# Kernel optimization log

Hardware: AMD Instinct MI355X
Metric: run time of the kernel (lower is better)

The kernel has to match this reference:

```python
import jax, jax.numpy as jnp
import numpy as np

ALPHA = 0.2  # LeakyReLU negative slope


def _gat_layer(h, dst, adj, w, a_in, a_out, b):
    # h: [N, F_in], dst: [N, K] int (edge (i,k): i -> dst[i,k]), adj: [N, K]
    hid = h @ w                      # [N, D]
    s_in = hid @ a_in                # [N]  (attention applied to source-node half)
    s_out = hid @ a_out              # [N]  (attention applied to dest-node half)
    # edge scores, grouped per source node (matches view(-1, num_neighs) softmax)
    e = jax.nn.leaky_relu(s_in[:, None] + s_out[dst], ALPHA)   # [N, K]
    # torch code detaches attention (Variable(..., requires_grad=False))
    att = jax.lax.stop_gradient(jax.nn.softmax(e, axis=1))     # [N, K]
    w_edge = adj * att                                          # [N, K]
    # SpMM: out[i] = sum_k w_edge[i,k] * hid[dst[i,k]]
    out = jnp.einsum('nk,nkd->nd', w_edge, hid[dst]) + b        # [N, D]
    return out


def setup_inputs() -> dict:
    key = jax.random.key(0)
    ks = jax.random.split(key, 12)
    N, K, F, H, O = 100000, 16, 128, 128, 128
    stdv1 = 1.0 / np.sqrt(H)
    stdv2 = 1.0 / np.sqrt(O)
    u = lambda k, shp, s: jax.random.uniform(k, shp, jnp.float32, -s, s)
    return {
        'x': jax.random.normal(ks[0], (N, F), jnp.float32),
        'dst_idx': jax.random.randint(ks[1], (N, K), 0, N),
        'adj_vals': jax.random.uniform(ks[2], (N, K), jnp.float32),
        'w1': u(ks[3], (F, H), stdv1),
        'a_in1': jax.random.normal(ks[4], (H,), jnp.float32) * (1.414 / np.sqrt(H)),
        'a_out1': jax.random.normal(ks[5], (H,), jnp.float32) * (1.414 / np.sqrt(H)),
        'b1': u(ks[6], (H,), stdv1),
        'w2': u(ks[7], (H, O), stdv2),
        'a_in2': jax.random.normal(ks[8], (O,), jnp.float32) * (1.414 / np.sqrt(O)),
        'a_out2': jax.random.normal(ks[9], (O,), jnp.float32) * (1.414 / np.sqrt(O)),
        'b2': u(ks[10], (O,), stdv2),
    }


def reference(x, dst_idx, adj_vals, w1, a_in1, a_out1, b1, w2, a_in2, a_out2, b2):
    h = jax.nn.relu(_gat_layer(x, dst_idx, adj_vals, w1, a_in1, a_out1, b1))
    h = jax.nn.relu(_gat_layer(h, dst_idx, adj_vals, w2, a_in2, a_out2, b2))
    return h
```

## Files before the change

### kernel.cpp

```cpp
#include <hip/hip_runtime.h>

#define ALPHA 0.2f
#define LDA 136

typedef short bf16x8 __attribute__((ext_vector_type(8)));
typedef float f32x4  __attribute__((ext_vector_type(4)));

static __device__ __forceinline__ float bf2f(unsigned short u) {
    union { unsigned int i; float f; } v; v.i = ((unsigned int)u) << 16; return v.f;
}
static __device__ __forceinline__ unsigned short f2bf(float f) {
    union { float f; unsigned int i; } v; v.f = f;
    unsigned int x = v.i;
    return (unsigned short)((x + 0x7fffu + ((x >> 16) & 1u)) >> 16);
}

__global__ __launch_bounds__(256)
void prep_wT_kernel(const float* __restrict__ w1, const float* __restrict__ w2,
                    unsigned short* __restrict__ wT1, unsigned short* __restrict__ wT2)
{
    __shared__ unsigned short wL[128 * 130];
    const float* w = blockIdx.x ? w2 : w1;
    unsigned short* wT = blockIdx.x ? wT2 : wT1;
    const int tid = threadIdx.x;

    for (int i = 0; i < 16; i++) {
        int e = tid + i * 256;
        int k = e >> 5, c0 = (e & 31) * 4;
        float4 v = *(const float4*)&w[k * 128 + c0];
        wL[(c0 + 0) * 130 + k] = f2bf(v.x);
        wL[(c0 + 1) * 130 + k] = f2bf(v.y);
        wL[(c0 + 2) * 130 + k] = f2bf(v.z);
        wL[(c0 + 3) * 130 + k] = f2bf(v.w);
    }
    __syncthreads();
    for (int i = 0; i < 8; i++) {
        int e = tid + i * 256;
        int c = e >> 4, k0 = (e & 15) * 8;
        ushort4 a, b;
        a.x = wL[c * 130 + k0 + 0]; a.y = wL[c * 130 + k0 + 1];
        a.z = wL[c * 130 + k0 + 2]; a.w = wL[c * 130 + k0 + 3];
        b.x = wL[c * 130 + k0 + 4]; b.y = wL[c * 130 + k0 + 5];
        b.z = wL[c * 130 + k0 + 6]; b.w = wL[c * 130 + k0 + 7];
        *(ushort4*)&wT[c * 128 + k0]     = a;
        *(ushort4*)&wT[c * 128 + k0 + 4] = b;
    }
}

template <bool SRC_BF>
__global__ __launch_bounds__(256)
void gemm_score_mfma(const void* __restrict__ srcv,
                     const unsigned short* __restrict__ wT,
                     const float* __restrict__ a_in,
                     const float* __restrict__ a_out,
                     unsigned short* __restrict__ hid,
                     float* __restrict__ s_in,
                     float* __restrict__ s_out,
                     int n)
{
    __shared__ short As[64 * LDA];
    __shared__ short Bs[128 * LDA];
    __shared__ float aS[2][128];

    const int tid = threadIdx.x;
    const int rbase = blockIdx.x * 64;

    if (tid < 128) { aS[0][tid] = a_in[tid]; aS[1][tid] = a_out[tid]; }

    if (SRC_BF) {
        const unsigned short* src = (const unsigned short*)srcv;
        #pragma unroll
        for (int i = 0; i < 8; i++) {
            int e = tid + i * 256;
            int r = e >> 5, c4 = (e & 31) * 4;
            int gr = rbase + r;
            ushort4 v;
            if (gr < n) v = *(const ushort4*)&src[(size_t)gr * 128 + c4];
            else { v.x = v.y = v.z = v.w = 0; }
            *(ushort4*)&As[r * LDA + c4] = v;
        }
    } else {
        const float* src = (const float*)srcv;
        #pragma unroll
        for (int i = 0; i < 8; i++) {
            int e = tid + i * 256;
            int r = e >> 5, c4 = (e & 31) * 4;
            int gr = rbase + r;
            ushort4 u;
            if (gr < n) {
                float4 v = *(const float4*)&src[(size_t)gr * 128 + c4];
                u.x = f2bf(v.x); u.y = f2bf(v.y); u.z = f2bf(v.z); u.w = f2bf(v.w);
            } else { u.x = u.y = u.z = u.w = 0; }
            *(ushort4*)&As[r * LDA + c4] = u;
        }
    }
    #pragma unroll
    for (int i = 0; i < 8; i++) {
        int e = tid + i * 256;
        int nr = e >> 4, j = (e & 15) * 8;
        int4 v = *(const int4*)&wT[nr * 128 + j];
        *(int4*)&Bs[nr * LDA + j] = v;
    }
    __syncthreads();

    const int lane = tid & 63;
    const int wv = tid >> 6;
    const int m = lane & 15;
    const int q = lane >> 4;

    f32x4 acc[8];
    #pragma unroll
    for (int t = 0; t < 8; t++) acc[t] = (f32x4){0.f, 0.f, 0.f, 0.f};

    const short* Abase = &As[(wv * 16 + m) * LDA + q * 8];
    const short* Bbase = &Bs[m * LDA + q * 8];

    #pragma unroll
    for (int ks = 0; ks < 4; ks++) {
        bf16x8 aF = *(const bf16x8*)(Abase + ks * 32);
        #pragma unroll
        for (int t = 0; t < 8; t++) {
            bf16x8 bF = *(const bf16x8*)(Bbase + t * 16 * LDA + ks * 32);
            acc[t] = __builtin_amdgcn_mfma_f32_16x16x32_bf16(aF, bF, acc[t], 0, 0, 0);
        }
    }

    float pin[4] = {0.f, 0.f, 0.f, 0.f}, pout[4] = {0.f, 0.f, 0.f, 0.f};
    #pragma unroll
    for (int t = 0; t < 8; t++) {
        float ai = aS[0][t * 16 + m];
        float ao = aS[1][t * 16 + m];
        #pragma unroll
        for (int r = 0; r < 4; r++) {
            pin[r]  += acc[t][r] * ai;
            pout[r] += acc[t][r] * ao;
        }
    }
    #pragma unroll
    for (int msk = 8; msk >= 1; msk >>= 1) {
        #pragma unroll
        for (int r = 0; r < 4; r++) {
            pin[r]  += __shfl_xor(pin[r],  msk);
            pout[r] += __shfl_xor(pout[r], msk);
        }
    }
    if (m == 0) {
        #pragma unroll
        for (int r = 0; r < 4; r++) {
            int g = rbase + wv * 16 + q * 4 + r;
            if (g < n) { s_in[g] = pin[r]; s_out[g] = pout[r]; }
        }
    }

    #pragma unroll
    for (int t = 0; t < 8; t++)
        #pragma unroll
        for (int r = 0; r < 4; r++)
            As[(wv * 16 + q * 4 + r) * LDA + t * 16 + m] = (short)f2bf(acc[t][r]);
    __syncthreads();
    #pragma unroll
    for (int i = 0; i < 4; i++) {
        int e = tid + i * 256;
        int r = e >> 4, j = (e & 15) * 8;
        int gr = rbase + r;
        if (gr < n) {
            int4 v = *(const int4*)&As[r * LDA + j];
            *(int4*)&hid[(size_t)gr * 128 + j] = v;
        }
    }
}

template <bool FINAL>
__global__ __launch_bounds__(256)
void gat_aggregate_kernel(const unsigned short* __restrict__ hid,
                          const float* __restrict__ s_in,
                          const float* __restrict__ s_out,
                          const int* __restrict__ dst,
                          const float* __restrict__ adj,
                          const float* __restrict__ bias,
                          void* __restrict__ outv,
                          int n)
{
    const int lane = threadIdx.x & 63;
    const int node = (blockIdx.x * 256 + threadIdx.x) >> 6;
    if (node >= n) return;

    float sc = -1e30f;
    int dk = 0;
    float av = 0.f;
    if (lane < 16) {
        int ei = node * 16 + lane;
        dk = dst[ei];
        av = adj[ei];
        float e = s_in[node] + s_out[dk];
        sc = (e > 0.f) ? e : ALPHA * e;
    }
    float m = sc;
    #pragma unroll
    for (int msk = 8; msk >= 1; msk >>= 1) m = fmaxf(m, __shfl_xor(m, msk));
    float p = (lane < 16) ? __expf(sc - m) : 0.f;
    float s = p;
    #pragma unroll
    for (int msk = 8; msk >= 1; msk >>= 1) s += __shfl_xor(s, msk);
    float wk = (lane < 16) ? av * p / s : 0.f;

    const int sub = lane >> 4;
    const int oct = lane & 15;
    int   gdk[4];
    float gwk[4];
    #pragma unroll
    for (int j = 0; j < 4; j++) {
        gdk[j] = __shfl(dk, 4 * j + sub);
        gwk[j] = __shfl(wk, 4 * j + sub);
    }

    float acc[8];
    #pragma unroll
    for (int i = 0; i < 8; i++) acc[i] = 0.f;
    #pragma unroll
    for (int j = 0; j < 4; j++) {
        bf16x8 hv = *(const bf16x8*)&hid[(size_t)gdk[j] * 128 + oct * 8];
        float wj = gwk[j];
        #pragma unroll
        for (int i = 0; i < 8; i++)
            acc[i] += wj * bf2f((unsigned short)hv[i]);
    }
    #pragma unroll
    for (int i = 0; i < 8; i++) {
        acc[i] += __shfl_xor(acc[i], 16);
        acc[i] += __shfl_xor(acc[i], 32);
    }

    if (lane < 16) {
        float4 b0 = *(const float4*)&bias[oct * 8];
        float4 b1 = *(const float4*)&bias[oct * 8 + 4];
        float o[8];
        o[0] = fmaxf(acc[0] + b0.x, 0.f); o[1] = fmaxf(acc[1] + b0.y, 0.f);
        o[2] = fmaxf(acc[2] + b0.z, 0.f); o[3] = fmaxf(acc[3] + b0.w, 0.f);
        o[4] = fmaxf(acc[4] + b1.x, 0.f); o[5] = fmaxf(acc[5] + b1.y, 0.f);
        o[6] = fmaxf(acc[6] + b1.z, 0.f); o[7] = fmaxf(acc[7] + b1.w, 0.f);

        const size_t obase = (size_t)node * 128 + oct * 8;
        if (FINAL) {
            float* of = (float*)outv;
            *(float4*)&of[obase]     = make_float4(o[0], o[1], o[2], o[3]);
            *(float4*)&of[obase + 4] = make_float4(o[4], o[5], o[6], o[7]);
        } else {
            unsigned short* oh = (unsigned short*)outv;
            ushort4 u0, u1;
            u0.x = f2bf(o[0]); u0.y = f2bf(o[1]); u0.z = f2bf(o[2]); u0.w = f2bf(o[3]);
            u1.x = f2bf(o[4]); u1.y = f2bf(o[5]); u1.z = f2bf(o[6]); u1.w = f2bf(o[7]);
            *(ushort4*)&oh[obase]     = u0;
            *(ushort4*)&oh[obase + 4] = u1;
        }
    }
}

extern "C" void kernel_launch(void* const* d_in, const int* in_sizes, int n_in,
                              void* d_out, int out_size, void* d_ws, size_t ws_size,
                              hipStream_t stream)
{
    const float* x      = (const float*)d_in[0];
    const int*   dst    = (const int*)d_in[1];
    const float* adj    = (const float*)d_in[2];
    const float* w1     = (const float*)d_in[3];
    const float* a_in1  = (const float*)d_in[4];
    const float* a_out1 = (const float*)d_in[5];
    const float* b1     = (const float*)d_in[6];
    const float* w2     = (const float*)d_in[7];
    const float* a_in2  = (const float*)d_in[8];
    const float* a_out2 = (const float*)d_in[9];
    const float* b2     = (const float*)d_in[10];

    const int N = in_sizes[0] / 128;

    unsigned short* hid   = (unsigned short*)d_ws;
    float*          s_in  = (float*)(hid + (size_t)N * 128);
    float*          s_out = s_in + N;
    unsigned short* wT1   = (unsigned short*)(s_out + N);
    unsigned short* wT2   = wT1 + 128 * 128;
    unsigned short* h1    = (unsigned short*)d_out + out_size;

    dim3 blk(256);
    dim3 ggrid((N + 63) / 64);
    dim3 agrid((N + 3) / 4);

    prep_wT_kernel<<<2, blk, 0, stream>>>(w1, w2, wT1, wT2);

    gemm_score_mfma<false><<<ggrid, blk, 0, stream>>>(x,  wT1, a_in1, a_out1,
                                                      hid, s_in, s_out, N);
    gat_aggregate_kernel<false><<<agrid, blk, 0, stream>>>(hid, s_in, s_out, dst,
                                                           adj, b1, h1, N);
    gemm_score_mfma<true><<<ggrid, blk, 0, stream>>>(h1, wT2, a_in2, a_out2,
                                                     hid, s_in, s_out, N);
    gat_aggregate_kernel<true><<<agrid, blk, 0, stream>>>(hid, s_in, s_out, dst,
                                                          adj, b2, d_out, N);
}
```

Before: 276.0 us.

## Load GEMM operands directly from global into MFMA registers, drop LDS staging

The GEMM kernel no longer stages the input rows and the transposed weight into shared memory. Each lane loads its A fragments straight from global memory into registers, and B fragments come from the small L2-resident weight buffer. This cuts LDS use from about 52KB to about 17KB per block, which allows higher occupancy and removes a barrier and the LDS round trip. The cost is redundant global/L2 reads of the weight by every wave. The weight transpose prep kernel is also rewritten to spread the work over 32 blocks without shared memory.

```diff
diff --git a/kernel.cpp b/kernel.cpp
--- a/kernel.cpp
+++ b/kernel.cpp
@@ -15,36 +15,23 @@
     return (unsigned short)((x + 0x7fffu + ((x >> 16) & 1u)) >> 16);
 }
 
-__global__ __launch_bounds__(256)
+__global__ __launch_bounds__(128)
 void prep_wT_kernel(const float* __restrict__ w1, const float* __restrict__ w2,
                     unsigned short* __restrict__ wT1, unsigned short* __restrict__ wT2)
 {
-    __shared__ unsigned short wL[128 * 130];
-    const float* w = blockIdx.x ? w2 : w1;
-    unsigned short* wT = blockIdx.x ? wT2 : wT1;
-    const int tid = threadIdx.x;
-
-    for (int i = 0; i < 16; i++) {
-        int e = tid + i * 256;
-        int k = e >> 5, c0 = (e & 31) * 4;
-        float4 v = *(const float4*)&w[k * 128 + c0];
-        wL[(c0 + 0) * 130 + k] = f2bf(v.x);
-        wL[(c0 + 1) * 130 + k] = f2bf(v.y);
-        wL[(c0 + 2) * 130 + k] = f2bf(v.z);
-        wL[(c0 + 3) * 130 + k] = f2bf(v.w);
-    }
-    __syncthreads();
-    for (int i = 0; i < 8; i++) {
-        int e = tid + i * 256;
-        int c = e >> 4, k0 = (e & 15) * 8;
-        ushort4 a, b;
-        a.x = wL[c * 130 + k0 + 0]; a.y = wL[c * 130 + k0 + 1];
-        a.z = wL[c * 130 + k0 + 2]; a.w = wL[c * 130 + k0 + 3];
-        b.x = wL[c * 130 + k0 + 4]; b.y = wL[c * 130 + k0 + 5];
-        b.z = wL[c * 130 + k0 + 6]; b.w = wL[c * 130 + k0 + 7];
-        *(ushort4*)&wT[c * 128 + k0]     = a;
-        *(ushort4*)&wT[c * 128 + k0 + 4] = b;
-    }
+    const int b = blockIdx.x;
+    const float* w = (b >> 4) ? w2 : w1;
+    unsigned short* wT = (b >> 4) ? wT2 : wT1;
+    const int k0 = (b & 15) * 8;
+    const int c = threadIdx.x;
+
+    ushort4 u0, u1;
+    u0.x = f2bf(w[(k0 + 0) * 128 + c]); u0.y = f2bf(w[(k0 + 1) * 128 + c]);
+    u0.z = f2bf(w[(k0 + 2) * 128 + c]); u0.w = f2bf(w[(k0 + 3) * 128 + c]);
+    u1.x = f2bf(w[(k0 + 4) * 128 + c]); u1.y = f2bf(w[(k0 + 5) * 128 + c]);
+    u1.z = f2bf(w[(k0 + 6) * 128 + c]); u1.w = f2bf(w[(k0 + 7) * 128 + c]);
+    *(ushort4*)&wT[c * 128 + k0]     = u0;
+    *(ushort4*)&wT[c * 128 + k0 + 4] = u1;
 }
 
 template <bool SRC_BF>
@@ -58,70 +45,57 @@
                      float* __restrict__ s_out,
                      int n)
 {
-    __shared__ short As[64 * LDA];
-    __shared__ short Bs[128 * LDA];
+    __shared__ short Es[64 * LDA];
     __shared__ float aS[2][128];
 
-    const int tid = threadIdx.x;
+    const int tid  = threadIdx.x;
+    const int lane = tid & 63;
+    const int wv   = tid >> 6;
+    const int m    = lane & 15;
+    const int q    = lane >> 4;
     const int rbase = blockIdx.x * 64;
+    const int row   = rbase + wv * 16 + m;
+    const bool rok  = (row < n);
 
     if (tid < 128) { aS[0][tid] = a_in[tid]; aS[1][tid] = a_out[tid]; }
-
+    __syncthreads();
+
+    bf16x8 aF[4];
     if (SRC_BF) {
         const unsigned short* src = (const unsigned short*)srcv;
-        #pragma unroll
-        for (int i = 0; i < 8; i++) {
-            int e = tid + i * 256;
-            int r = e >> 5, c4 = (e & 31) * 4;
-            int gr = rbase + r;
-            ushort4 v;
-            if (gr < n) v = *(const ushort4*)&src[(size_t)gr * 128 + c4];
-            else { v.x = v.y = v.z = v.w = 0; }
-            *(ushort4*)&As[r * LDA + c4] = v;
-        }
+        const unsigned short* p = &src[(size_t)row * 128 + q * 8];
+        #pragma unroll
+        for (int ks = 0; ks < 4; ks++)
+            aF[ks] = rok ? *(const bf16x8*)(p + ks * 32) : (bf16x8){0,0,0,0,0,0,0,0};
     } else {
         const float* src = (const float*)srcv;
-        #pragma unroll
-        for (int i = 0; i < 8; i++) {
-            int e = tid + i * 256;
-            int r = e >> 5, c4 = (e & 31) * 4;
-            int gr = rbase + r;
-            ushort4 u;
-            if (gr < n) {
-                float4 v = *(const float4*)&src[(size_t)gr * 128 + c4];
-                u.x = f2bf(v.x); u.y = f2bf(v.y); u.z = f2bf(v.z); u.w = f2bf(v.w);
-            } else { u.x = u.y = u.z = u.w = 0; }
-            *(ushort4*)&As[r * LDA + c4] = u;
-        }
-    }
-    #pragma unroll
-    for (int i = 0; i < 8; i++) {
-        int e = tid + i * 256;
-        int nr = e >> 4, j = (e & 15) * 8;
-        int4 v = *(const int4*)&wT[nr * 128 + j];
-        *(int4*)&Bs[nr * LDA + j] = v;
-    }
-    __syncthreads();
-
-    const int lane = tid & 63;
-    const int wv = tid >> 6;
-    const int m = lane & 15;
-    const int q = lane >> 4;
+        const float* p = &src[(size_t)row * 128 + q * 8];
+        #pragma unroll
+        for (int ks = 0; ks < 4; ks++) {
+            if (rok) {
+                float4 v0 = *(const float4*)(p + ks * 32);
+                float4 v1 = *(const float4*)(p + ks * 32 + 4);
+                bf16x8 a;
+                a[0] = (short)f2bf(v0.x); a[1] = (short)f2bf(v0.y);
+                a[2] = (short)f2bf(v0.z); a[3] = (short)f2bf(v0.w);
+                a[4] = (short)f2bf(v1.x); a[5] = (short)f2bf(v1.y);
+                a[6] = (short)f2bf(v1.z); a[7] = (short)f2bf(v1.w);
+                aF[ks] = a;
+            } else aF[ks] = (bf16x8){0,0,0,0,0,0,0,0};
+        }
+    }
 
     f32x4 acc[8];
     #pragma unroll
     for (int t = 0; t < 8; t++) acc[t] = (f32x4){0.f, 0.f, 0.f, 0.f};
 
-    const short* Abase = &As[(wv * 16 + m) * LDA + q * 8];
-    const short* Bbase = &Bs[m * LDA + q * 8];
-
-    #pragma unroll
-    for (int ks = 0; ks < 4; ks++) {
-        bf16x8 aF = *(const bf16x8*)(Abase + ks * 32);
-        #pragma unroll
-        for (int t = 0; t < 8; t++) {
-            bf16x8 bF = *(const bf16x8*)(Bbase + t * 16 * LDA + ks * 32);
-            acc[t] = __builtin_amdgcn_mfma_f32_16x16x32_bf16(aF, bF, acc[t], 0, 0, 0);
+    const unsigned short* Bp = &wT[m * 128 + q * 8];
+    #pragma unroll
+    for (int t = 0; t < 8; t++) {
+        #pragma unroll
+        for (int ks = 0; ks < 4; ks++) {
+            bf16x8 bF = *(const bf16x8*)(Bp + ((size_t)t * 16 * 128) + ks * 32);
+            acc[t] = __builtin_amdgcn_mfma_f32_16x16x32_bf16(aF[ks], bF, acc[t], 0, 0, 0);
         }
     }
 
@@ -156,7 +130,7 @@
     for (int t = 0; t < 8; t++)
         #pragma unroll
         for (int r = 0; r < 4; r++)
-            As[(wv * 16 + q * 4 + r) * LDA + t * 16 + m] = (short)f2bf(acc[t][r]);
+            Es[(wv * 16 + q * 4 + r) * LDA + t * 16 + m] = (short)f2bf(acc[t][r]);
     __syncthreads();
     #pragma unroll
     for (int i = 0; i < 4; i++) {
@@ -164,7 +138,7 @@
         int r = e >> 4, j = (e & 15) * 8;
         int gr = rbase + r;
         if (gr < n) {
-            int4 v = *(const int4*)&As[r * LDA + j];
+            int4 v = *(const int4*)&Es[r * LDA + j];
             *(int4*)&hid[(size_t)gr * 128 + j] = v;
         }
     }
@@ -285,7 +259,7 @@
     dim3 ggrid((N + 63) / 64);
     dim3 agrid((N + 3) / 4);
 
-    prep_wT_kernel<<<2, blk, 0, stream>>>(w1, w2, wT1, wT2);
+    prep_wT_kernel<<<32, 128, 0, stream>>>(w1, w2, wT1, wT2);
 
     gemm_score_mfma<false><<<ggrid, blk, 0, stream>>>(x,  wT1, a_in1, a_out1,
                                                       hid, s_in, s_out, N);
```

Measured after the change: 304.7 us. 10.4% more time.
